# Optimization experiments

Hardware: AMD Instinct MI355X
Metric: run time of the kernel (lower is better)

The kernel has to match this reference:

```python
import jax, jax.numpy as jnp
import numpy as np

BN_EPS = 1e-5

def setup_inputs() -> dict:
    key = jax.random.key(0)
    ks = jax.random.split(key, 16)
    B, H, W, C = 4, 64, 64, 256
    N = H * W                      # 4096 tokens
    heads, sr = 8, 2
    Nk = (H // sr) * (W // sr)     # 1024 reduced KV tokens
    s = 0.02
    return {
        "x": jax.random.normal(ks[0], (B, N, C), jnp.float32),
        "H": H,
        "W": W,
        "relative_pos": jax.random.normal(ks[1], (heads, N, Nk), jnp.float32),
        # linear weights, torch layout [out, in]; q/k/v have no bias (qkv_bias=False)
        "q_w": jax.random.normal(ks[2], (C, C), jnp.float32) * s,
        "k_w": jax.random.normal(ks[3], (C, C), jnp.float32) * s,
        "v_w": jax.random.normal(ks[4], (C, C), jnp.float32) * s,
        "proj_w": jax.random.normal(ks[5], (C, C), jnp.float32) * s,
        "proj_b": jnp.zeros((C,), jnp.float32),
        # depthwise conv (groups=C): OIHW with I=1
        "sr_w": jax.random.normal(ks[6], (C, 1, sr, sr), jnp.float32) * s,
        "sr_b": jnp.zeros((C,), jnp.float32),
        # BatchNorm2d (eval mode) params/buffers
        "bn_gamma": jnp.ones((C,), jnp.float32),
        "bn_beta": jnp.zeros((C,), jnp.float32),
        "bn_mean": jax.random.normal(ks[7], (C,), jnp.float32) * 0.1,
        "bn_var": jax.random.uniform(ks[8], (C,), jnp.float32, 0.5, 1.5),
    }


def reference(x, H, W, relative_pos, q_w, k_w, v_w, proj_w, proj_b,
              sr_w, sr_b, bn_gamma, bn_beta, bn_mean, bn_var):
    B, N, C = x.shape
    heads = relative_pos.shape[0]
    qk_dim = q_w.shape[0]
    dh = qk_dim // heads
    dv = C // heads
    scale = dh ** -0.5
    sr = sr_w.shape[-1]

    # q: [B, heads, N, dh]
    q = (x @ q_w.T).reshape(B, N, heads, dh).transpose(0, 2, 1, 3)

    # spatial reduction: depthwise conv stride sr + BatchNorm (eval)
    x_img = x.transpose(0, 2, 1).reshape(B, C, H, W)
    xk = jax.lax.conv_general_dilated(
        x_img, sr_w, window_strides=(sr, sr), padding='VALID',
        feature_group_count=C,
        dimension_numbers=('NCHW', 'OIHW', 'NCHW')) + sr_b[None, :, None, None]
    inv_std = bn_gamma / jnp.sqrt(bn_var + BN_EPS)
    xk = (xk - bn_mean[None, :, None, None]) * inv_std[None, :, None, None] \
         + bn_beta[None, :, None, None]
    Nk = xk.shape[2] * xk.shape[3]
    xk = xk.reshape(B, C, Nk).transpose(0, 2, 1)   # [B, Nk, C]

    k = (xk @ k_w.T).reshape(B, Nk, heads, dh).transpose(0, 2, 1, 3)
    v = (xk @ v_w.T).reshape(B, Nk, heads, dv).transpose(0, 2, 1, 3)

    # scores + additive relative position bias, softmax, weighted sum
    attn = jnp.einsum('bhnd,bhmd->bhnm', q, k) * scale + relative_pos[None]
    attn = jax.nn.softmax(attn, axis=-1)
    out = jnp.einsum('bhnm,bhmd->bhnd', attn, v)
    out = out.transpose(0, 2, 1, 3).reshape(B, N, C)
    return out @ proj_w.T + proj_b
```

## Files before the change

kernel.cpp:

```cpp
#include <hip/hip_runtime.h>
#include <cstdint>
#include <cstddef>

#define DEV static __device__ __forceinline__

typedef __bf16 bf16x8 __attribute__((ext_vector_type(8)));
typedef __bf16 bf16x4 __attribute__((ext_vector_type(4)));
typedef float  f32x4  __attribute__((ext_vector_type(4)));
typedef unsigned short us4 __attribute__((ext_vector_type(4)));
typedef unsigned int   u32x4 __attribute__((ext_vector_type(4)));

DEV unsigned short f2bf(float f) {
  unsigned u = __float_as_uint(f);
  u += 0x7FFFu + ((u >> 16) & 1u);
  return (unsigned short)(u >> 16);
}

constexpr int   Bn = 4, Nn = 4096, Cn = 256, HEADSn = 8, DHn = 32, NKn = 1024;
constexpr float SCALEc = 0.17677669529663689f;
constexpr float L2E    = 1.4426950408889634f;

__global__ void k_f32_to_bf16(const float* __restrict__ src,
                              unsigned short* __restrict__ dst, int n4, float scale) {
  int i = blockIdx.x * blockDim.x + threadIdx.x;
  if (i < n4) {
    f32x4 v = *(const f32x4*)(src + 4 * (size_t)i);
    us4 o;
    o[0] = f2bf(v[0] * scale); o[1] = f2bf(v[1] * scale);
    o[2] = f2bf(v[2] * scale); o[3] = f2bf(v[3] * scale);
    *(us4*)(dst + 4 * (size_t)i) = o;
  }
}

__global__ void k_conv_bn(const float* __restrict__ x,
                          const float* __restrict__ srw, const float* __restrict__ srb,
                          const float* __restrict__ bng, const float* __restrict__ bnb,
                          const float* __restrict__ bnm, const float* __restrict__ bnv,
                          unsigned short* __restrict__ xk) {
  const int m = blockIdx.x;
  const int b = blockIdx.y;
  const int c = threadIdx.x;
  const int i = m >> 5, j = m & 31;
  const int n00 = (2 * i) * 64 + 2 * j;
  const size_t base = ((size_t)b * Nn) * Cn + c;
  float w0 = srw[c * 4 + 0], w1 = srw[c * 4 + 1], w2 = srw[c * 4 + 2], w3 = srw[c * 4 + 3];
  float acc = x[base + (size_t)n00 * Cn] * w0
            + x[base + (size_t)(n00 + 1) * Cn] * w1
            + x[base + (size_t)(n00 + 64) * Cn] * w2
            + x[base + (size_t)(n00 + 65) * Cn] * w3
            + srb[c];
  float inv_std = bng[c] * rsqrtf(bnv[c] + 1e-5f);
  acc = (acc - bnm[c]) * inv_std + bnb[c];
  xk[((size_t)b * NKn + m) * Cn + c] = f2bf(acc);
}

template <int MODE>
__global__ __launch_bounds__(256) void k_gemm(const unsigned short* __restrict__ A,
                                              const unsigned short* __restrict__ W,
                                              void* __restrict__ outp,
                                              const float* __restrict__ bias, int rs) {
  __shared__ __align__(16) unsigned short sA[64 * 256];
  __shared__ __align__(16) unsigned short sW[64 * 256];
  const int tid = threadIdx.x;
  const int lane = tid & 63, w = tid >> 6;
  const int g = lane >> 4, c = lane & 15;
  const int m0 = blockIdx.x * 64, o0 = blockIdx.y * 64;

#pragma unroll
  for (int r = 0; r < 8; ++r) {
    const int row = r * 8 + (tid >> 5);
    const int u = tid & 31;
    const int usw = u ^ (row & 7);
    bf16x8 va = *(const bf16x8*)(A + (size_t)(m0 + row) * Cn + u * 8);
    *(bf16x8*)(sA + row * Cn + usw * 8) = va;
    bf16x8 vw = *(const bf16x8*)(W + (size_t)(o0 + row) * Cn + u * 8);
    *(bf16x8*)(sW + row * Cn + usw * 8) = vw;
  }
  __syncthreads();

  f32x4 acc[4] = {};
  const int rowa = w * 16 + c;
#pragma unroll
  for (int ks = 0; ks < 8; ++ks) {
    bf16x8 af = *(const bf16x8*)(sA + rowa * Cn + ((ks * 4 + g) ^ (c & 7)) * 8);
#pragma unroll
    for (int t = 0; t < 4; ++t) {
      const int roww = 16 * t + c;
      bf16x8 wf = *(const bf16x8*)(sW + roww * Cn + ((ks * 4 + g) ^ (c & 7)) * 8);
      acc[t] = __builtin_amdgcn_mfma_f32_16x16x32_bf16(af, wf, acc[t], 0, 0, 0);
    }
  }

  const int mb = m0 + w * 16;
  if (MODE == 0) {
    unsigned short* ob = (unsigned short*)outp;
#pragma unroll
    for (int t = 0; t < 4; ++t)
#pragma unroll
      for (int r = 0; r < 4; ++r)
        ob[(size_t)(mb + 4 * g + r) * Cn + o0 + 16 * t + c] = f2bf(acc[t][r]);
  } else if (MODE == 1) {
    unsigned short* vt = (unsigned short*)outp;
    const int m4 = mb + 4 * g;
    const int b = m4 >> 10;
    const int kvblk = (m4 & 1023) >> 5;
    const int jh = (m4 >> 4) & 1;
#pragma unroll
    for (int t = 0; t < 4; ++t) {
      const int o = o0 + 16 * t + c;
      const int h = o >> 5, dv = o & 31;
      us4 pk;
      pk[0] = f2bf(acc[t][0]); pk[1] = f2bf(acc[t][1]);
      pk[2] = f2bf(acc[t][2]); pk[3] = f2bf(acc[t][3]);
      *(us4*)(vt + ((size_t)(((b * 8 + h) * 32 + kvblk) * 32 + dv)) * 32 + g * 8 + jh * 4) = pk;
    }
  } else if (MODE == 2) {
    float* of = (float*)outp;
#pragma unroll
    for (int t = 0; t < 4; ++t) {
      const int o = o0 + 16 * t + c;
      const float bv = bias[o];
#pragma unroll
      for (int r = 0; r < 4; ++r)
        of[(size_t)(mb + 4 * g + r) * Cn + o] = acc[t][r] + bv;
    }
  } else {
    unsigned short* ot = (unsigned short*)outp;
#pragma unroll
    for (int t = 0; t < 4; ++t) {
      const int o = o0 + 16 * t + c;
      const int h = o >> 5, dh = o & 31;
#pragma unroll
      for (int r = 0; r < 4; ++r) {
        const int m = mb + 4 * g + r;
        const int b = m >> rs, rl = m & ((1 << rs) - 1);
        ot[((size_t)(((b * 8 + h) << rs) + rl)) * 32 + dh] = f2bf(acc[t][r]);
      }
    }
  }
}

__global__ __launch_bounds__(256, 2) void k_attn(const unsigned short* __restrict__ qt,
                                                 const unsigned short* __restrict__ kt,
                                                 const unsigned short* __restrict__ vt,
                                                 const float* __restrict__ rel,
                                                 unsigned short* __restrict__ ob) {
  __shared__ __align__(16) char s_rel[2][16384];
  const int tid = threadIdx.x;
  const int lane = tid & 63, bb = tid >> 6;
  const int g = lane >> 4, c = lane & 15;
  const int h = blockIdx.x >> 5;
  const int q0 = (blockIdx.x & 31) * 128;

  const int srow = tid >> 1, sub4 = (tid & 1) * 4;
  const float* sgp = rel + ((size_t)h * Nn + q0 + srow) * NKn + sub4 * 4;
  int swo[4];
#pragma unroll
  for (int j = 0; j < 4; ++j) swo[j] = srow * 128 + (((sub4 + j) ^ (srow & 7)) << 4);
  char* sb = &s_rel[0][0];

  bf16x8 qf[8];
#pragma unroll
  for (int t = 0; t < 8; ++t)
    qf[t] = *(const bf16x8*)(qt + ((size_t)((bb * 8 + h) << 12) + q0 + 16 * t + c) * 32 + 8 * g);

  bf16x8 ones;
#pragma unroll
  for (int r = 0; r < 8; ++r) ones[r] = (__bf16)1.0f;

  f32x4 acc[8][2] = {};
  f32x4 accl[8] = {};

  const unsigned short* kbase = kt + ((size_t)((bb * 8 + h) << 10)) * 32 + 8 * g;
  const unsigned short* vbase = vt + ((size_t)(bb * 8 + h) * 1024) * 32;

  auto sub = [&](const char* rb, int t, bf16x8 k0, bf16x8 k1, bf16x8 v0, bf16x8 v1) {
    f32x4 zero = {};
    f32x4 s0 = __builtin_amdgcn_mfma_f32_16x16x32_bf16(k0, qf[t], zero, 0, 0, 0);
    f32x4 s1 = __builtin_amdgcn_mfma_f32_16x16x32_bf16(k1, qf[t], zero, 0, 0, 0);
    const int rrow = (16 * t + c) * 128;
    f32x4 r0 = *(const f32x4*)(rb + rrow + ((g ^ (c & 7)) << 4));
    f32x4 r1 = *(const f32x4*)(rb + rrow + (((4 + g) ^ (c & 7)) << 4));
    s0 += r0 * L2E;
    s1 += r1 * L2E;
    float p0[4], p1[4];
#pragma unroll
    for (int r = 0; r < 4; ++r) {
      p0[r] = __builtin_amdgcn_exp2f(s0[r]);
      p1[r] = __builtin_amdgcn_exp2f(s1[r]);
    }
    u32x4 pw;
    pw[0] = __builtin_amdgcn_perm(__float_as_uint(p0[1]), __float_as_uint(p0[0]), 0x07060302u);
    pw[1] = __builtin_amdgcn_perm(__float_as_uint(p0[3]), __float_as_uint(p0[2]), 0x07060302u);
    pw[2] = __builtin_amdgcn_perm(__float_as_uint(p1[1]), __float_as_uint(p1[0]), 0x07060302u);
    pw[3] = __builtin_amdgcn_perm(__float_as_uint(p1[3]), __float_as_uint(p1[2]), 0x07060302u);
    bf16x8 pf = __builtin_bit_cast(bf16x8, pw);
    accl[t] = __builtin_amdgcn_mfma_f32_16x16x32_bf16(ones, pf, accl[t], 0, 0, 0);
    acc[t][0] = __builtin_amdgcn_mfma_f32_16x16x32_bf16(v0, pf, acc[t][0], 0, 0, 0);
    acc[t][1] = __builtin_amdgcn_mfma_f32_16x16x32_bf16(v1, pf, acc[t][1], 0, 0, 0);
  };

  auto tile = [&](int e, int rbuf,
                  bf16x8& k0c, bf16x8& k1c, bf16x8& v0c, bf16x8& v1c,
                  bf16x8& k0n, bf16x8& k1n, bf16x8& v0n, bf16x8& v1n,
                  f32x4& S0, f32x4& S1, f32x4& S2, f32x4& S3) {
    char* wb = sb + (rbuf ^ 1) * 16384;
    *(f32x4*)(wb + swo[0]) = S0;
    *(f32x4*)(wb + swo[1]) = S1;
    *(f32x4*)(wb + swo[2]) = S2;
    *(f32x4*)(wb + swo[3]) = S3;
    const int kvn = ((e + 1) & 31) * 32;
    k0n = *(const bf16x8*)(kbase + (size_t)(kvn + c) * 32);
    k1n = *(const bf16x8*)(kbase + (size_t)(kvn + 16 + c) * 32);
    v0n = *(const bf16x8*)(vbase + (size_t)(kvn + c) * 32 + g * 8);
    v1n = *(const bf16x8*)(vbase + (size_t)(kvn + 16 + c) * 32 + g * 8);
    __builtin_amdgcn_sched_barrier(0);
    const char* rb = sb + rbuf * 16384;
#pragma unroll
    for (int t = 0; t < 8; ++t) sub(rb, t, k0c, k1c, v0c, v1c);
    const int rn = ((e + 3) & 31) * 32;
    S0 = *(const f32x4*)(sgp + rn);
    S1 = *(const f32x4*)(sgp + rn + 4);
    S2 = *(const f32x4*)(sgp + rn + 8);
    S3 = *(const f32x4*)(sgp + rn + 12);
  };

  {
    f32x4 t0 = *(const f32x4*)(sgp);
    f32x4 t1 = *(const f32x4*)(sgp + 4);
    f32x4 t2 = *(const f32x4*)(sgp + 8);
    f32x4 t3 = *(const f32x4*)(sgp + 12);
    *(f32x4*)(sb + swo[0]) = t0;
    *(f32x4*)(sb + swo[1]) = t1;
    *(f32x4*)(sb + swo[2]) = t2;
    *(f32x4*)(sb + swo[3]) = t3;
  }
  f32x4 SA0 = *(const f32x4*)(sgp + 32);
  f32x4 SA1 = *(const f32x4*)(sgp + 36);
  f32x4 SA2 = *(const f32x4*)(sgp + 40);
  f32x4 SA3 = *(const f32x4*)(sgp + 44);
  f32x4 SB0 = *(const f32x4*)(sgp + 64);
  f32x4 SB1 = *(const f32x4*)(sgp + 68);
  f32x4 SB2 = *(const f32x4*)(sgp + 72);
  f32x4 SB3 = *(const f32x4*)(sgp + 76);
  bf16x8 kP0 = *(const bf16x8*)(kbase + (size_t)(c) * 32);
  bf16x8 kP1 = *(const bf16x8*)(kbase + (size_t)(16 + c) * 32);
  bf16x8 vP0 = *(const bf16x8*)(vbase + (size_t)(c) * 32 + g * 8);
  bf16x8 vP1 = *(const bf16x8*)(vbase + (size_t)(16 + c) * 32 + g * 8);
  bf16x8 kQ0, kQ1, vQ0, vQ1;
  __syncthreads();

  for (int ee = 0; ee < 32; ee += 2) {
    tile(ee, 0, kP0, kP1, vP0, vP1, kQ0, kQ1, vQ0, vQ1, SA0, SA1, SA2, SA3);
    __syncthreads();
    tile(ee + 1, 1, kQ0, kQ1, vQ0, vQ1, kP0, kP1, vP0, vP1, SB0, SB1, SB2, SB3);
    __syncthreads();
  }

#pragma unroll
  for (int t = 0; t < 8; ++t) {
    const float inv = 1.0f / accl[t][0];
#pragma unroll
    for (int hh = 0; hh < 2; ++hh) {
      us4 pk;
      pk[0] = f2bf(acc[t][hh][0] * inv);
      pk[1] = f2bf(acc[t][hh][1] * inv);
      pk[2] = f2bf(acc[t][hh][2] * inv);
      pk[3] = f2bf(acc[t][hh][3] * inv);
      *(us4*)(ob + ((size_t)bb * Nn + q0 + 16 * t + c) * Cn + h * DHn + hh * 16 + 4 * g) = pk;
    }
  }
}

extern "C" void kernel_launch(void* const* d_in, const int* in_sizes, int n_in,
                              void* d_out, int out_size, void* d_ws, size_t ws_size,
                              hipStream_t stream) {
  const float* x   = (const float*)d_in[0];
  const float* rel = (const float*)d_in[3];
  const float* qw  = (const float*)d_in[4];
  const float* kw  = (const float*)d_in[5];
  const float* vw  = (const float*)d_in[6];
  const float* pw  = (const float*)d_in[7];
  const float* pb  = (const float*)d_in[8];
  const float* srw = (const float*)d_in[9];
  const float* srb = (const float*)d_in[10];
  const float* bng = (const float*)d_in[11];
  const float* bnb = (const float*)d_in[12];
  const float* bnm = (const float*)d_in[13];
  const float* bnv = (const float*)d_in[14];

  char* ws = (char*)d_ws;
  unsigned short* x_bf  = (unsigned short*)(ws + 0);
  unsigned short* q_t   = (unsigned short*)(ws + 8388608);
  unsigned short* xk_bf = (unsigned short*)(ws + 16777216);
  unsigned short* k_t   = (unsigned short*)(ws + 18874368);
  unsigned short* v_2   = (unsigned short*)(ws + 20971520);
  unsigned short* a_bf  = (unsigned short*)(ws + 23068672);
  unsigned short* w_q   = (unsigned short*)(ws + 31457280);
  unsigned short* w_k   = (unsigned short*)(ws + 31457280 + 131072);
  unsigned short* w_v   = (unsigned short*)(ws + 31457280 + 262144);
  unsigned short* w_p   = (unsigned short*)(ws + 31457280 + 393216);

  k_f32_to_bf16<<<4096, 256, 0, stream>>>(x, x_bf, 1048576, 1.0f);
  k_f32_to_bf16<<<64, 256, 0, stream>>>(qw, w_q, 16384, SCALEc * L2E);
  k_f32_to_bf16<<<64, 256, 0, stream>>>(kw, w_k, 16384, 1.0f);
  k_f32_to_bf16<<<64, 256, 0, stream>>>(vw, w_v, 16384, 1.0f);
  k_f32_to_bf16<<<64, 256, 0, stream>>>(pw, w_p, 16384, 1.0f);

  k_conv_bn<<<dim3(1024, 4), 256, 0, stream>>>(x, srw, srb, bng, bnb, bnm, bnv, xk_bf);

  k_gemm<3><<<dim3(256, 4), 256, 0, stream>>>(x_bf, w_q, (void*)q_t, nullptr, 12);
  k_gemm<3><<<dim3(64, 4), 256, 0, stream>>>(xk_bf, w_k, (void*)k_t, nullptr, 10);
  k_gemm<1><<<dim3(64, 4), 256, 0, stream>>>(xk_bf, w_v, (void*)v_2, nullptr, 0);

  k_attn<<<dim3(256), 256, 0, stream>>>(q_t, k_t, v_2, rel, a_bf);

  k_gemm<2><<<dim3(256, 4), 256, 0, stream>>>(a_bf, w_p, d_out, pb, 0);
}
```

Measured before the change: 85.51 us.

## Split attention block query rows across two wave groups with 512 threads

Doubles the attention block from 256 to 512 threads. Each wave now handles one batch and one half of the block's 128 query rows, so it holds 4 query tiles instead of 8, and the relative-position staging is split across twice as many threads. The aim is more waves per CU to hide latency of the relative-position stream and the exp work, with fewer registers per wave. The cost is that K/V fragments are loaded twice per block, once by each query half, and block-wide barriers now synchronise more waves.

```diff
diff --git a/kernel.cpp b/kernel.cpp
--- a/kernel.cpp
+++ b/kernel.cpp
@@ -140,36 +140,37 @@
   }
 }
 
-__global__ __launch_bounds__(256, 2) void k_attn(const unsigned short* __restrict__ qt,
+__global__ __launch_bounds__(512, 2) void k_attn(const unsigned short* __restrict__ qt,
                                                  const unsigned short* __restrict__ kt,
                                                  const unsigned short* __restrict__ vt,
                                                  const float* __restrict__ rel,
                                                  unsigned short* __restrict__ ob) {
   __shared__ __align__(16) char s_rel[2][16384];
   const int tid = threadIdx.x;
-  const int lane = tid & 63, bb = tid >> 6;
+  const int lane = tid & 63, w = tid >> 6;
+  const int bb = w & 3, qh = w >> 2;
   const int g = lane >> 4, c = lane & 15;
   const int h = blockIdx.x >> 5;
   const int q0 = (blockIdx.x & 31) * 128;
 
-  const int srow = tid >> 1, sub4 = (tid & 1) * 4;
-  const float* sgp = rel + ((size_t)h * Nn + q0 + srow) * NKn + sub4 * 4;
-  int swo[4];
-#pragma unroll
-  for (int j = 0; j < 4; ++j) swo[j] = srow * 128 + (((sub4 + j) ^ (srow & 7)) << 4);
+  const int srow = tid >> 2, su2 = (tid & 3) * 2;
+  const float* sgp = rel + ((size_t)h * Nn + q0 + srow) * NKn + su2 * 4;
+  int swo[2];
+#pragma unroll
+  for (int j = 0; j < 2; ++j) swo[j] = srow * 128 + (((su2 + j) ^ (srow & 7)) << 4);
   char* sb = &s_rel[0][0];
 
-  bf16x8 qf[8];
-#pragma unroll
-  for (int t = 0; t < 8; ++t)
-    qf[t] = *(const bf16x8*)(qt + ((size_t)((bb * 8 + h) << 12) + q0 + 16 * t + c) * 32 + 8 * g);
+  bf16x8 qf[4];
+#pragma unroll
+  for (int t = 0; t < 4; ++t)
+    qf[t] = *(const bf16x8*)(qt + ((size_t)((bb * 8 + h) << 12) + q0 + qh * 64 + 16 * t + c) * 32 + 8 * g);
 
   bf16x8 ones;
 #pragma unroll
   for (int r = 0; r < 8; ++r) ones[r] = (__bf16)1.0f;
 
-  f32x4 acc[8][2] = {};
-  f32x4 accl[8] = {};
+  f32x4 acc[4][2] = {};
+  f32x4 accl[4] = {};
 
   const unsigned short* kbase = kt + ((size_t)((bb * 8 + h) << 10)) * 32 + 8 * g;
   const unsigned short* vbase = vt + ((size_t)(bb * 8 + h) * 1024) * 32;
@@ -178,7 +179,7 @@
     f32x4 zero = {};
     f32x4 s0 = __builtin_amdgcn_mfma_f32_16x16x32_bf16(k0, qf[t], zero, 0, 0, 0);
     f32x4 s1 = __builtin_amdgcn_mfma_f32_16x16x32_bf16(k1, qf[t], zero, 0, 0, 0);
-    const int rrow = (16 * t + c) * 128;
+    const int rrow = (qh * 64 + 16 * t + c) * 128;
     f32x4 r0 = *(const f32x4*)(rb + rrow + ((g ^ (c & 7)) << 4));
     f32x4 r1 = *(const f32x4*)(rb + rrow + (((4 + g) ^ (c & 7)) << 4));
     s0 += r0 * L2E;
@@ -203,12 +204,10 @@
   auto tile = [&](int e, int rbuf,
                   bf16x8& k0c, bf16x8& k1c, bf16x8& v0c, bf16x8& v1c,
                   bf16x8& k0n, bf16x8& k1n, bf16x8& v0n, bf16x8& v1n,
-                  f32x4& S0, f32x4& S1, f32x4& S2, f32x4& S3) {
+                  f32x4& S0, f32x4& S1) {
     char* wb = sb + (rbuf ^ 1) * 16384;
     *(f32x4*)(wb + swo[0]) = S0;
     *(f32x4*)(wb + swo[1]) = S1;
-    *(f32x4*)(wb + swo[2]) = S2;
-    *(f32x4*)(wb + swo[3]) = S3;
     const int kvn = ((e + 1) & 31) * 32;
     k0n = *(const bf16x8*)(kbase + (size_t)(kvn + c) * 32);
     k1n = *(const bf16x8*)(kbase + (size_t)(kvn + 16 + c) * 32);
@@ -217,32 +216,22 @@
     __builtin_amdgcn_sched_barrier(0);
     const char* rb = sb + rbuf * 16384;
 #pragma unroll
-    for (int t = 0; t < 8; ++t) sub(rb, t, k0c, k1c, v0c, v1c);
+    for (int t = 0; t < 4; ++t) sub(rb, t, k0c, k1c, v0c, v1c);
     const int rn = ((e + 3) & 31) * 32;
     S0 = *(const f32x4*)(sgp + rn);
     S1 = *(const f32x4*)(sgp + rn + 4);
-    S2 = *(const f32x4*)(sgp + rn + 8);
-    S3 = *(const f32x4*)(sgp + rn + 12);
   };
 
   {
     f32x4 t0 = *(const f32x4*)(sgp);
     f32x4 t1 = *(const f32x4*)(sgp + 4);
-    f32x4 t2 = *(const f32x4*)(sgp + 8);
-    f32x4 t3 = *(const f32x4*)(sgp + 12);
     *(f32x4*)(sb + swo[0]) = t0;
     *(f32x4*)(sb + swo[1]) = t1;
-    *(f32x4*)(sb + swo[2]) = t2;
-    *(f32x4*)(sb + swo[3]) = t3;
   }
   f32x4 SA0 = *(const f32x4*)(sgp + 32);
   f32x4 SA1 = *(const f32x4*)(sgp + 36);
-  f32x4 SA2 = *(const f32x4*)(sgp + 40);
-  f32x4 SA3 = *(const f32x4*)(sgp + 44);
   f32x4 SB0 = *(const f32x4*)(sgp + 64);
   f32x4 SB1 = *(const f32x4*)(sgp + 68);
-  f32x4 SB2 = *(const f32x4*)(sgp + 72);
-  f32x4 SB3 = *(const f32x4*)(sgp + 76);
   bf16x8 kP0 = *(const bf16x8*)(kbase + (size_t)(c) * 32);
   bf16x8 kP1 = *(const bf16x8*)(kbase + (size_t)(16 + c) * 32);
   bf16x8 vP0 = *(const bf16x8*)(vbase + (size_t)(c) * 32 + g * 8);
@@ -251,14 +240,14 @@
   __syncthreads();
 
   for (int ee = 0; ee < 32; ee += 2) {
-    tile(ee, 0, kP0, kP1, vP0, vP1, kQ0, kQ1, vQ0, vQ1, SA0, SA1, SA2, SA3);
+    tile(ee, 0, kP0, kP1, vP0, vP1, kQ0, kQ1, vQ0, vQ1, SA0, SA1);
     __syncthreads();
-    tile(ee + 1, 1, kQ0, kQ1, vQ0, vQ1, kP0, kP1, vP0, vP1, SB0, SB1, SB2, SB3);
+    tile(ee + 1, 1, kQ0, kQ1, vQ0, vQ1, kP0, kP1, vP0, vP1, SB0, SB1);
     __syncthreads();
   }
 
 #pragma unroll
-  for (int t = 0; t < 8; ++t) {
+  for (int t = 0; t < 4; ++t) {
     const float inv = 1.0f / accl[t][0];
 #pragma unroll
     for (int hh = 0; hh < 2; ++hh) {
@@ -267,7 +256,7 @@
       pk[1] = f2bf(acc[t][hh][1] * inv);
       pk[2] = f2bf(acc[t][hh][2] * inv);
       pk[3] = f2bf(acc[t][hh][3] * inv);
-      *(us4*)(ob + ((size_t)bb * Nn + q0 + 16 * t + c) * Cn + h * DHn + hh * 16 + 4 * g) = pk;
+      *(us4*)(ob + ((size_t)bb * Nn + q0 + qh * 64 + 16 * t + c) * Cn + h * DHn + hh * 16 + 4 * g) = pk;
     }
   }
 }
@@ -313,7 +302,7 @@
   k_gemm<3><<<dim3(64, 4), 256, 0, stream>>>(xk_bf, w_k, (void*)k_t, nullptr, 10);
   k_gemm<1><<<dim3(64, 4), 256, 0, stream>>>(xk_bf, w_v, (void*)v_2, nullptr, 0);
 
-  k_attn<<<dim3(256), 256, 0, stream>>>(q_t, k_t, v_2, rel, a_bf);
+  k_attn<<<dim3(256), 512, 0, stream>>>(q_t, k_t, v_2, rel, a_bf);
 
   k_gemm<2><<<dim3(256, 4), 256, 0, stream>>>(a_bf, w_p, d_out, pb, 0);
 }
```

After: 80.87 us. -5.4%, faster.
